# Optimization experiments

Measured on AMD Instinct MI355X. Metric: run time of the kernel, lower is better.

## Reference

```python
import jax, jax.numpy as jnp
import numpy as np

N_NODES = 100000


def setup_inputs() -> dict:
    key = jax.random.key(0)
    k1, k2, k3, k4, k5, k6 = jax.random.split(key, 6)
    n_edges = 1600000
    X = jax.random.normal(k1, (N_NODES, 256), dtype=jnp.float32)
    edge_row = jax.random.randint(k2, (n_edges,), 0, N_NODES, dtype=jnp.int64)
    edge_col = jax.random.randint(k3, (n_edges,), 0, N_NODES, dtype=jnp.int64)
    edge_val = jax.random.uniform(k4, (n_edges,), dtype=jnp.float32)
    W = jax.random.normal(k5, (128, 256), dtype=jnp.float32) * 0.05
    b = jax.random.normal(k6, (128,), dtype=jnp.float32) * 0.05
    return {"X": X, "edge_row": edge_row, "edge_col": edge_col,
            "edge_val": edge_val, "W": W, "b": b}


def reference(X, edge_row, edge_col, edge_val, W, b):
    # Dense projection: H = X @ W^T + b  -> [N, out_dim]
    H = jnp.einsum('ni,oi->no', X, W) + b
    # SpMM: out[r] = sum_e A[r, c_e] * H[c_e] over edges with row r
    msgs = edge_val[:, None] * H[edge_col]          # [E, out_dim]
    out = jax.ops.segment_sum(msgs, edge_row, num_segments=N_NODES)
    return out
```

## Files before the change

kernel.cpp:

```cpp
#include <hip/hip_runtime.h>
#include <hip/hip_bf16.h>

#define NNODES 100000
#define NEDGES 1600000
#define KDIM 256
#define ODIM 128
#define NB_SCAN 98
#define EDGE_CAP 1900032
#define ESTRIDE 400000
#define GEMM_BLOCKS 1563
#define RANK_BLOCKS 1563

typedef __attribute__((ext_vector_type(8))) short short8;
typedef __attribute__((ext_vector_type(4))) float floatx4;

static __device__ __forceinline__ short f2bf(float f) {
  union { float f; unsigned u; } x; x.f = f;
  unsigned r = (x.u + 0x7fffu + ((x.u >> 16) & 1u)) >> 16;
  return (short)r;
}

__global__ void conv_w_kernel(const float* __restrict__ W, short* __restrict__ Wb) {
  int i = blockIdx.x * 256 + threadIdx.x;
  if (i < ODIM * KDIM) Wb[i] = f2bf(W[i]);
}

__global__ void scan1_kernel(const int* __restrict__ counts, int* __restrict__ chunkExcl,
                             int* __restrict__ blockSums) {
  __shared__ int s[256];
  int t = threadIdx.x;
  int base = blockIdx.x * 1024 + t * 4;
  int v[4];
#pragma unroll
  for (int j = 0; j < 4; j++) {
    int idx = base + j;
    v[j] = (idx < NNODES) ? ((counts[idx] + 3) & ~3) : 0;
  }
  int sum = v[0] + v[1] + v[2] + v[3];
  s[t] = sum;
  __syncthreads();
  for (int o = 1; o < 256; o <<= 1) {
    int add = (t >= o) ? s[t - o] : 0;
    __syncthreads();
    s[t] += add;
    __syncthreads();
  }
  int run = s[t] - sum;
#pragma unroll
  for (int j = 0; j < 4; j++) {
    int idx = base + j;
    if (idx < NNODES) chunkExcl[idx] = run;
    run += v[j];
  }
  if (t == 255) blockSums[blockIdx.x] = s[255];
}

__global__ void scan2_kernel(const int* __restrict__ blockSums, int* __restrict__ blockBase,
                             int* __restrict__ offsets) {
  __shared__ int s[128];
  int t = threadIdx.x;
  int v = (t < NB_SCAN) ? blockSums[t] : 0;
  s[t] = v;
  __syncthreads();
  for (int o = 1; o < 128; o <<= 1) {
    int add = (t >= o) ? s[t - o] : 0;
    __syncthreads();
    s[t] += add;
    __syncthreads();
  }
  if (t < NB_SCAN) blockBase[t] = s[t] - v;
  if (t == 127) offsets[NNODES] = s[127];
}

__global__ void scan3_kernel(const int* __restrict__ chunkExcl, const int* __restrict__ blockBase,
                             int* __restrict__ offsets) {
  int i = blockIdx.x * 256 + threadIdx.x;
  if (i < NNODES) offsets[i] = chunkExcl[i] + blockBase[i >> 10];
}

__global__ void place_kernel(const int* __restrict__ rows, const int* __restrict__ cols,
                             const float* __restrict__ vals,
                             const unsigned short* __restrict__ rank,
                             const int* __restrict__ offsets, int2* __restrict__ edges) {
  int i = blockIdx.x * 256 + threadIdx.x;
#pragma unroll
  for (int j = 0; j < 4; j++) {
    int e = i + j * ESTRIDE;
    if (e < NEDGES) {
      int r = rows[e];
      int p = offsets[r] + (int)rank[e];
      int2 rec;
      rec.x = cols[e];
      rec.y = __float_as_int(vals[e]);
      edges[p] = rec;
    }
  }
}

__global__ __launch_bounds__(256) void gemm_rank_kernel(
    const float* __restrict__ X, const short* __restrict__ Wb,
    const float* __restrict__ bias, unsigned short* __restrict__ H,
    const int* __restrict__ rows, int* __restrict__ counts,
    unsigned short* __restrict__ rank) {
  if (blockIdx.x >= GEMM_BLOCKS) {
    int i = (blockIdx.x - GEMM_BLOCKS) * 256 + threadIdx.x;
#pragma unroll
    for (int j = 0; j < 4; j++) {
      int e = i + j * ESTRIDE;
      if (e < NEDGES) {
        int r = rows[e];
        rank[e] = (unsigned short)atomicAdd(&counts[r], 1);
      }
    }
    return;
  }
  const int lane = threadIdx.x & 63;
  const int wave = threadIdx.x >> 6;
  const int l16 = lane & 15;
  const int quad = lane >> 4;
  const int rowBase = blockIdx.x * 64 + wave * 16;
  const int arow = rowBase + l16;
  const bool inb = arow < NNODES;
  const float4 zf4 = {0.f, 0.f, 0.f, 0.f};
  const float4* xp = (const float4*)(X + (size_t)(inb ? arow : 0) * KDIM + quad * 8);

  floatx4 acc[8];
#pragma unroll
  for (int t = 0; t < 8; t++) acc[t] = (floatx4){0.f, 0.f, 0.f, 0.f};

  float4 c0 = inb ? xp[0] : zf4;
  float4 c1 = inb ? xp[1] : zf4;
#pragma unroll
  for (int k0 = 0; k0 < 8; k0++) {
    float4 n0, n1;
    if (k0 < 7) {
      n0 = inb ? xp[(k0 + 1) * 8] : zf4;
      n1 = inb ? xp[(k0 + 1) * 8 + 1] : zf4;
    }
    short8 a;
    a[0] = f2bf(c0.x); a[1] = f2bf(c0.y); a[2] = f2bf(c0.z); a[3] = f2bf(c0.w);
    a[4] = f2bf(c1.x); a[5] = f2bf(c1.y); a[6] = f2bf(c1.z); a[7] = f2bf(c1.w);
    const short* bp = Wb + k0 * 32 + quad * 8;
#pragma unroll
    for (int t = 0; t < 8; t++) {
      short8 b = *(const short8*)(bp + (size_t)(t * 16 + l16) * KDIM);
      acc[t] = __builtin_amdgcn_mfma_f32_16x16x32_bf16(a, b, acc[t], 0, 0, 0);
    }
    if (k0 < 7) { c0 = n0; c1 = n1; }
  }

#pragma unroll
  for (int t = 0; t < 8; t++) {
    const int col = t * 16 + l16;
    const float bv = bias[col];
#pragma unroll
    for (int r = 0; r < 4; r++) {
      const int row = rowBase + quad * 4 + r;
      if (row < NNODES) H[(size_t)row * ODIM + col] = (unsigned short)f2bf(acc[t][r] + bv);
    }
  }
}

__global__ __launch_bounds__(256) void spmm_kernel(const int* __restrict__ offsets,
                                                   const int2* __restrict__ edges,
                                                   const unsigned* __restrict__ H2,
                                                   float* __restrict__ out) {
  const int lane = threadIdx.x & 63;
  const int row = blockIdx.x * 4 + (threadIdx.x >> 6);
  if (row >= NNODES) return;
  const int s = offsets[row];
  const int e = offsets[row + 1];
  float ax = 0.f, ay = 0.f;
  for (int i = s; i < e; i += 4) {
    const int4 p01 = *(const int4*)(edges + i);
    const int4 p23 = *(const int4*)(edges + i + 2);
    const unsigned h0 = H2[(size_t)p01.x * 64 + lane];
    const unsigned h1 = H2[(size_t)p01.z * 64 + lane];
    const unsigned h2 = H2[(size_t)p23.x * 64 + lane];
    const unsigned h3 = H2[(size_t)p23.z * 64 + lane];
    const float v0 = __int_as_float(p01.y);
    const float v1 = __int_as_float(p01.w);
    const float v2 = __int_as_float(p23.y);
    const float v3 = __int_as_float(p23.w);
    ax += v0 * __uint_as_float(h0 << 16);
    ay += v0 * __uint_as_float(h0 & 0xffff0000u);
    ax += v1 * __uint_as_float(h1 << 16);
    ay += v1 * __uint_as_float(h1 & 0xffff0000u);
    ax += v2 * __uint_as_float(h2 << 16);
    ay += v2 * __uint_as_float(h2 & 0xffff0000u);
    ax += v3 * __uint_as_float(h3 << 16);
    ay += v3 * __uint_as_float(h3 & 0xffff0000u);
  }
  float2 r;
  r.x = ax;
  r.y = ay;
  ((float2*)out)[(size_t)row * 64 + lane] = r;
}

extern "C" void kernel_launch(void* const* d_in, const int* in_sizes, int n_in,
                              void* d_out, int out_size, void* d_ws, size_t ws_size,
                              hipStream_t stream) {
  const float* X = (const float*)d_in[0];
  const int* erow = (const int*)d_in[1];
  const int* ecol = (const int*)d_in[2];
  const float* eval = (const float*)d_in[3];
  const float* W = (const float*)d_in[4];
  const float* bias = (const float*)d_in[5];
  float* out = (float*)d_out;

  char* ws = (char*)d_ws;
  size_t off = 0;
  auto alloc = [&](size_t bytes) -> char* {
    char* p = ws + off;
    off += (bytes + 255) & ~(size_t)255;
    return p;
  };
  unsigned short* Hb = (unsigned short*)alloc((size_t)NNODES * ODIM * 2);
  short* Wb = (short*)alloc((size_t)ODIM * KDIM * 2);
  int* counts = (int*)alloc((size_t)NNODES * 4);
  int* chunkExcl = (int*)alloc((size_t)NNODES * 4);
  int* offsets = (int*)alloc((size_t)(NNODES + 1) * 4);
  int* blockSums = (int*)alloc((size_t)NB_SCAN * 4);
  int* blockBase = (int*)alloc((size_t)NB_SCAN * 4);
  unsigned short* rank = (unsigned short*)alloc((size_t)NEDGES * 2);
  int2* edges = (int2*)alloc((size_t)EDGE_CAP * 8);

  hipMemsetAsync(counts, 0, (size_t)NNODES * 4, stream);
  hipMemsetAsync(edges, 0, (size_t)EDGE_CAP * 8, stream);
  conv_w_kernel<<<(ODIM * KDIM + 255) / 256, 256, 0, stream>>>(W, Wb);
  gemm_rank_kernel<<<GEMM_BLOCKS + RANK_BLOCKS, 256, 0, stream>>>(X, Wb, bias, Hb,
                                                                 erow, counts, rank);
  scan1_kernel<<<NB_SCAN, 256, 0, stream>>>(counts, chunkExcl, blockSums);
  scan2_kernel<<<1, 128, 0, stream>>>(blockSums, blockBase, offsets);
  scan3_kernel<<<(NNODES + 255) / 256, 256, 0, stream>>>(chunkExcl, blockBase, offsets);
  place_kernel<<<(ESTRIDE + 255) / 256, 256, 0, stream>>>(erow, ecol, eval, rank, offsets, edges);
  spmm_kernel<<<(NNODES + 3) / 4, 256, 0, stream>>>(offsets, edges, (const unsigned*)Hb, out);
}
```

Before: 386.4 us.

## Shard per-row edge counters to cut atomic contention; reshape H packing

Row counters are split into 16 shards per row, chosen by edge index low bits, so atomics in the rank pass contend less. The scan now sums the shards and writes per-shard base offsets back into the counts array, which the place kernel uses. The GEMM now loads all X rows up front and packs columns c and c+64 into one 32-bit word, so the SpMM writes two coalesced float rows instead of float2. The cost is a 16x larger counts buffer to memset and scan, and a bigger scan hierarchy.

New measurement: 437.8 us. 13.3% more time.

```diff
diff --git a/kernel.cpp b/kernel.cpp
--- a/kernel.cpp
+++ b/kernel.cpp
@@ -5,7 +5,8 @@
 #define NEDGES 1600000
 #define KDIM 256
 #define ODIM 128
-#define NB_SCAN 98
+#define NSHARD 16
+#define NB_SCAN 391
 #define EDGE_CAP 1900032
 #define ESTRIDE 400000
 #define GEMM_BLOCKS 1563
@@ -29,14 +30,15 @@
                              int* __restrict__ blockSums) {
   __shared__ int s[256];
   int t = threadIdx.x;
-  int base = blockIdx.x * 1024 + t * 4;
-  int v[4];
-#pragma unroll
-  for (int j = 0; j < 4; j++) {
-    int idx = base + j;
-    v[j] = (idx < NNODES) ? ((counts[idx] + 3) & ~3) : 0;
-  }
-  int sum = v[0] + v[1] + v[2] + v[3];
+  int n = blockIdx.x * 256 + t;
+  int sum = 0;
+  if (n < NNODES) {
+    const int4* c4 = (const int4*)(counts + (size_t)n * NSHARD);
+    int4 a = c4[0], b = c4[1], c = c4[2], d = c4[3];
+    sum = a.x + a.y + a.z + a.w + b.x + b.y + b.z + b.w +
+          c.x + c.y + c.z + c.w + d.x + d.y + d.z + d.w;
+    sum = (sum + 3) & ~3;
+  }
   s[t] = sum;
   __syncthreads();
   for (int o = 1; o < 256; o <<= 1) {
@@ -45,50 +47,58 @@
     s[t] += add;
     __syncthreads();
   }
-  int run = s[t] - sum;
-#pragma unroll
-  for (int j = 0; j < 4; j++) {
-    int idx = base + j;
-    if (idx < NNODES) chunkExcl[idx] = run;
-    run += v[j];
-  }
+  if (n < NNODES) chunkExcl[n] = s[t] - sum;
   if (t == 255) blockSums[blockIdx.x] = s[255];
 }
 
 __global__ void scan2_kernel(const int* __restrict__ blockSums, int* __restrict__ blockBase,
                              int* __restrict__ offsets) {
-  __shared__ int s[128];
+  __shared__ int s[512];
   int t = threadIdx.x;
   int v = (t < NB_SCAN) ? blockSums[t] : 0;
   s[t] = v;
   __syncthreads();
-  for (int o = 1; o < 128; o <<= 1) {
+  for (int o = 1; o < 512; o <<= 1) {
     int add = (t >= o) ? s[t - o] : 0;
     __syncthreads();
     s[t] += add;
     __syncthreads();
   }
   if (t < NB_SCAN) blockBase[t] = s[t] - v;
-  if (t == 127) offsets[NNODES] = s[127];
+  if (t == 511) offsets[NNODES] = s[511];
 }
 
 __global__ void scan3_kernel(const int* __restrict__ chunkExcl, const int* __restrict__ blockBase,
-                             int* __restrict__ offsets) {
-  int i = blockIdx.x * 256 + threadIdx.x;
-  if (i < NNODES) offsets[i] = chunkExcl[i] + blockBase[i >> 10];
+                             int* __restrict__ counts, int* __restrict__ offsets) {
+  int n = blockIdx.x * 256 + threadIdx.x;
+  if (n >= NNODES) return;
+  int run = chunkExcl[n] + blockBase[n >> 8];
+  offsets[n] = run;
+  int4* c4 = (int4*)(counts + (size_t)n * NSHARD);
+  int4 q0 = c4[0], q1 = c4[1], q2 = c4[2], q3 = c4[3];
+  int4 b0, b1, b2, b3;
+  b0.x = run; run += q0.x; b0.y = run; run += q0.y;
+  b0.z = run; run += q0.z; b0.w = run; run += q0.w;
+  b1.x = run; run += q1.x; b1.y = run; run += q1.y;
+  b1.z = run; run += q1.z; b1.w = run; run += q1.w;
+  b2.x = run; run += q2.x; b2.y = run; run += q2.y;
+  b2.z = run; run += q2.z; b2.w = run; run += q2.w;
+  b3.x = run; run += q3.x; b3.y = run; run += q3.y;
+  b3.z = run; run += q3.z; b3.w = run; run += q3.w;
+  c4[0] = b0; c4[1] = b1; c4[2] = b2; c4[3] = b3;
 }
 
 __global__ void place_kernel(const int* __restrict__ rows, const int* __restrict__ cols,
                              const float* __restrict__ vals,
                              const unsigned short* __restrict__ rank,
-                             const int* __restrict__ offsets, int2* __restrict__ edges) {
+                             const int* __restrict__ sbase, int2* __restrict__ edges) {
   int i = blockIdx.x * 256 + threadIdx.x;
 #pragma unroll
   for (int j = 0; j < 4; j++) {
     int e = i + j * ESTRIDE;
     if (e < NEDGES) {
       int r = rows[e];
-      int p = offsets[r] + (int)rank[e];
+      int p = sbase[(r << 4) | (e & 15)] + (int)rank[e];
       int2 rec;
       rec.x = cols[e];
       rec.y = __float_as_int(vals[e]);
@@ -99,7 +109,7 @@
 
 __global__ __launch_bounds__(256) void gemm_rank_kernel(
     const float* __restrict__ X, const short* __restrict__ Wb,
-    const float* __restrict__ bias, unsigned short* __restrict__ H,
+    const float* __restrict__ bias, unsigned* __restrict__ H2,
     const int* __restrict__ rows, int* __restrict__ counts,
     unsigned short* __restrict__ rank) {
   if (blockIdx.x >= GEMM_BLOCKS) {
@@ -109,7 +119,7 @@
       int e = i + j * ESTRIDE;
       if (e < NEDGES) {
         int r = rows[e];
-        rank[e] = (unsigned short)atomicAdd(&counts[r], 1);
+        rank[e] = (unsigned short)atomicAdd(&counts[(r << 4) | (e & 15)], 1);
       }
     }
     return;
@@ -124,19 +134,21 @@
   const float4 zf4 = {0.f, 0.f, 0.f, 0.f};
   const float4* xp = (const float4*)(X + (size_t)(inb ? arow : 0) * KDIM + quad * 8);
 
+  float4 xr[16];
+#pragma unroll
+  for (int k0 = 0; k0 < 8; k0++) {
+    xr[2 * k0]     = inb ? xp[k0 * 8]     : zf4;
+    xr[2 * k0 + 1] = inb ? xp[k0 * 8 + 1] : zf4;
+  }
+
   floatx4 acc[8];
 #pragma unroll
   for (int t = 0; t < 8; t++) acc[t] = (floatx4){0.f, 0.f, 0.f, 0.f};
 
-  float4 c0 = inb ? xp[0] : zf4;
-  float4 c1 = inb ? xp[1] : zf4;
 #pragma unroll
   for (int k0 = 0; k0 < 8; k0++) {
-    float4 n0, n1;
-    if (k0 < 7) {
-      n0 = inb ? xp[(k0 + 1) * 8] : zf4;
-      n1 = inb ? xp[(k0 + 1) * 8 + 1] : zf4;
-    }
+    const float4 c0 = xr[2 * k0];
+    const float4 c1 = xr[2 * k0 + 1];
     short8 a;
     a[0] = f2bf(c0.x); a[1] = f2bf(c0.y); a[2] = f2bf(c0.z); a[3] = f2bf(c0.w);
     a[4] = f2bf(c1.x); a[5] = f2bf(c1.y); a[6] = f2bf(c1.z); a[7] = f2bf(c1.w);
@@ -146,17 +158,21 @@
       short8 b = *(const short8*)(bp + (size_t)(t * 16 + l16) * KDIM);
       acc[t] = __builtin_amdgcn_mfma_f32_16x16x32_bf16(a, b, acc[t], 0, 0, 0);
     }
-    if (k0 < 7) { c0 = n0; c1 = n1; }
-  }
-
-#pragma unroll
-  for (int t = 0; t < 8; t++) {
-    const int col = t * 16 + l16;
-    const float bv = bias[col];
+  }
+
+#pragma unroll
+  for (int t = 0; t < 4; t++) {
+    const int cl = t * 16 + l16;
+    const float blo = bias[cl];
+    const float bhi = bias[cl + 64];
 #pragma unroll
     for (int r = 0; r < 4; r++) {
       const int row = rowBase + quad * 4 + r;
-      if (row < NNODES) H[(size_t)row * ODIM + col] = (unsigned short)f2bf(acc[t][r] + bv);
+      if (row < NNODES) {
+        unsigned lo = (unsigned short)f2bf(acc[t][r] + blo);
+        unsigned hi = (unsigned short)f2bf(acc[t + 4][r] + bhi);
+        H2[(size_t)row * 64 + cl] = lo | (hi << 16);
+      }
     }
   }
 }
@@ -191,10 +207,8 @@
     ax += v3 * __uint_as_float(h3 << 16);
     ay += v3 * __uint_as_float(h3 & 0xffff0000u);
   }
-  float2 r;
-  r.x = ax;
-  r.y = ay;
-  ((float2*)out)[(size_t)row * 64 + lane] = r;
+  out[(size_t)row * 128 + lane] = ax;
+  out[(size_t)row * 128 + 64 + lane] = ay;
 }
 
 extern "C" void kernel_launch(void* const* d_in, const int* in_sizes, int n_in,
@@ -215,9 +229,9 @@
     off += (bytes + 255) & ~(size_t)255;
     return p;
   };
-  unsigned short* Hb = (unsigned short*)alloc((size_t)NNODES * ODIM * 2);
+  unsigned* Hb = (unsigned*)alloc((size_t)NNODES * 64 * 4);
   short* Wb = (short*)alloc((size_t)ODIM * KDIM * 2);
-  int* counts = (int*)alloc((size_t)NNODES * 4);
+  int* counts = (int*)alloc((size_t)NNODES * NSHARD * 4);
   int* chunkExcl = (int*)alloc((size_t)NNODES * 4);
   int* offsets = (int*)alloc((size_t)(NNODES + 1) * 4);
   int* blockSums = (int*)alloc((size_t)NB_SCAN * 4);
@@ -225,14 +239,14 @@
   unsigned short* rank = (unsigned short*)alloc((size_t)NEDGES * 2);
   int2* edges = (int2*)alloc((size_t)EDGE_CAP * 8);
 
-  hipMemsetAsync(counts, 0, (size_t)NNODES * 4, stream);
+  hipMemsetAsync(counts, 0, (size_t)NNODES * NSHARD * 4, stream);
   hipMemsetAsync(edges, 0, (size_t)EDGE_CAP * 8, stream);
   conv_w_kernel<<<(ODIM * KDIM + 255) / 256, 256, 0, stream>>>(W, Wb);
   gemm_rank_kernel<<<GEMM_BLOCKS + RANK_BLOCKS, 256, 0, stream>>>(X, Wb, bias, Hb,
                                                                  erow, counts, rank);
   scan1_kernel<<<NB_SCAN, 256, 0, stream>>>(counts, chunkExcl, blockSums);
-  scan2_kernel<<<1, 128, 0, stream>>>(blockSums, blockBase, offsets);
-  scan3_kernel<<<(NNODES + 255) / 256, 256, 0, stream>>>(chunkExcl, blockBase, offsets);
-  place_kernel<<<(ESTRIDE + 255) / 256, 256, 0, stream>>>(erow, ecol, eval, rank, offsets, edges);
+  scan2_kernel<<<1, 512, 0, stream>>>(blockSums, blockBase, offsets);
+  scan3_kernel<<<NB_SCAN, 256, 0, stream>>>(chunkExcl, blockBase, counts, offsets);
+  place_kernel<<<(ESTRIDE + 255) / 256, 256, 0, stream>>>(erow, ecol, eval, rank, counts, edges);
   spmm_kernel<<<(NNODES + 3) / 4, 256, 0, stream>>>(offsets, edges, (const unsigned*)Hb, out);
 }
```
